# Kernel tuning notes

Measured on AMD Instinct MI355X. Metric: run time of the kernel, lower is better.

## Reference

```python
import jax, jax.numpy as jnp
import numpy as np

B, N, NPOINT, NSAMPLE = 8, 8192, 2048, 64
RADIUS = 0.2
C_IN = 64  # input feature channels; mlp[0]=64 -> 67 after use_xyz concat


def setup_inputs() -> dict:
    key = jax.random.key(0)
    ks = jax.random.split(key, 12)
    xyz = jax.random.uniform(ks[0], (B, N, 3), dtype=jnp.float32)
    features = jax.random.normal(ks[1], (B, N, C_IN), dtype=jnp.float32)
    inds = jax.random.randint(ks[2], (B, NPOINT), 0, N, dtype=jnp.int32)

    def mkw(k, cin, cout):
        return jax.random.normal(k, (cin, cout), jnp.float32) * (1.0 / np.sqrt(cin).astype(np.float32))

    w0 = mkw(ks[3], C_IN + 3, 64)
    w1 = mkw(ks[4], 64, 64)
    w2 = mkw(ks[5], 64, 128)
    # BN (inference) folded into per-channel scale/shift
    s0 = 1.0 + 0.1 * jax.random.normal(ks[6], (64,), jnp.float32)
    t0 = 0.1 * jax.random.normal(ks[7], (64,), jnp.float32)
    s1 = 1.0 + 0.1 * jax.random.normal(ks[8], (64,), jnp.float32)
    t1 = 0.1 * jax.random.normal(ks[9], (64,), jnp.float32)
    s2 = 1.0 + 0.1 * jax.random.normal(ks[10], (128,), jnp.float32)
    t2 = 0.1 * jax.random.normal(ks[11], (128,), jnp.float32)
    return dict(xyz=xyz, features=features, inds=inds,
                w0=w0, s0=s0, t0=t0, w1=w1, s1=s1, t1=t1, w2=w2, s2=s2, t2=t2)


def _ball_query(xyz, new_xyz):
    """First NSAMPLE point indices within RADIUS of each query; pad by repeating
    the first hit (matches CUDA ball_query semantics). xyz:(B,N,3) new_xyz:(B,S,3)."""
    nn = jnp.sum(xyz * xyz, axis=-1)            # (B,N)
    qq = jnp.sum(new_xyz * new_xyz, axis=-1)    # (B,S)
    d2 = qq[:, :, None] + nn[:, None, :] - 2.0 * jnp.einsum('bsc,bnc->bsn', new_xyz, xyz)
    within = d2 < (RADIUS * RADIUS)
    ar = jnp.arange(N, dtype=jnp.int32)
    keyed = jnp.where(within, ar[None, None, :], N)   # out-of-radius -> sentinel N
    keyed = jnp.sort(keyed, axis=-1)[:, :, :NSAMPLE]  # first hits in point order
    idx = jnp.where(keyed == N, keyed[:, :, :1], keyed)
    return jnp.minimum(idx, N - 1)


_gather = jax.vmap(lambda pts, i: pts[i])  # (N,C),(M,) -> (M,C) per batch


def reference(xyz, features, inds, w0, s0, t0, w1, s1, t1, w2, s2, t2):
    new_xyz = _gather(xyz, inds)                              # (B,S,3)
    idx = _ball_query(xyz, new_xyz)                           # (B,S,ns)
    flat = idx.reshape(B, NPOINT * NSAMPLE)
    g_xyz = _gather(xyz, flat).reshape(B, NPOINT, NSAMPLE, 3)
    g_xyz = (g_xyz - new_xyz[:, :, None, :]) / RADIUS         # normalize_xyz
    g_feat = _gather(features, flat).reshape(B, NPOINT, NSAMPLE, C_IN)
    x = jnp.concatenate([g_xyz, g_feat], axis=-1)             # (B,S,ns,C+3)
    for wgt, s, t in ((w0, s0, t0), (w1, s1, t1), (w2, s2, t2)):
        x = jax.nn.relu(jnp.einsum('bpsc,cd->bpsd', x, wgt) * s + t)
    new_features = jnp.max(x, axis=2)                         # max-pool over nsample
    return new_xyz, new_features, inds, idx
```

## Files before the change

kernel.cpp:

```cpp
#include <hip/hip_runtime.h>

#define BB 8
#define NN 8192
#define NPOINT 2048
#define NSAMPLE 64
#define CIN 64
#define RADIUS 0.2f
#define R2 (RADIUS * RADIUS)

#define OFF_NEWXYZ 0
#define OFF_FEAT (BB * NPOINT * 3)
#define OFF_INDS (OFF_FEAT + BB * NPOINT * 128)
#define OFF_IDX (OFF_INDS + BB * NPOINT)

typedef _Float16 half8 __attribute__((ext_vector_type(8)));
typedef _Float16 half4 __attribute__((ext_vector_type(4)));
typedef __fp16 f16x2 __attribute__((ext_vector_type(2)));
typedef float floatx16 __attribute__((ext_vector_type(16)));

#define P0 88
#define P1 72
#define X_LOC 0
#define H_LOC (64 * P0)
#define XH_WAVE (64 * P0 + 64 * P1)
#define WT0_S 0
#define WT1_S (64 * P0)
#define WT2_S (64 * P0 + 64 * P1)

#define QPW 8

__global__ __launch_bounds__(256) void ballq_kernel(
    const float* __restrict__ xyz, const int* __restrict__ inds,
    float* __restrict__ out) {
  __shared__ int sidx[4][2][NSAMPLE];
  const int wave = (blockIdx.x * 256 + threadIdx.x) >> 6;
  const int lane = threadIdx.x & 63;
  const int wid = threadIdx.x >> 6;
  const int q0 = wave * 2, q1 = q0 + 1;
  const int b = q0 >> 11;

  const float* xb = xyz + (size_t)b * NN * 3;
  const int i0 = inds[q0], i1 = inds[q1];
  const float c0x = xb[i0 * 3 + 0], c0y = xb[i0 * 3 + 1], c0z = xb[i0 * 3 + 2];
  const float c1x = xb[i1 * 3 + 0], c1y = xb[i1 * 3 + 1], c1z = xb[i1 * 3 + 2];

  if (lane < 2) {
    const int qq_ = lane ? q1 : q0;
    const int ii = lane ? i1 : i0;
    out[OFF_NEWXYZ + (size_t)qq_ * 3 + 0] = lane ? c1x : c0x;
    out[OFF_NEWXYZ + (size_t)qq_ * 3 + 1] = lane ? c1y : c0y;
    out[OFF_NEWXYZ + (size_t)qq_ * 3 + 2] = lane ? c1z : c0z;
    out[OFF_INDS + qq_] = (float)ii;
  }

  const float qq0 = c0x * c0x + c0y * c0y + c0z * c0z;
  const float qq1 = c1x * c1x + c1y * c1y + c1z * c1z;

  int cnt0 = 0, cnt1 = 0;
  float ax[4], ay[4], az[4];
#pragma unroll
  for (int k = 0; k < 4; ++k) {
    const float* p = xb + (size_t)(k * 64 + lane) * 3;
    ax[k] = p[0];
    ay[k] = p[1];
    az[k] = p[2];
  }
  for (int j0 = 0; j0 < NN; j0 += 256) {
    float bx[4] = {0}, by[4] = {0}, bz[4] = {0};
    const int jn = j0 + 256;
    if (jn < NN) {
#pragma unroll
      for (int k = 0; k < 4; ++k) {
        const float* p = xb + (size_t)(jn + k * 64 + lane) * 3;
        bx[k] = p[0];
        by[k] = p[1];
        bz[k] = p[2];
      }
    }
#pragma unroll
    for (int k = 0; k < 4; ++k) {
      const int j = j0 + k * 64 + lane;
      const float nn_ = ax[k] * ax[k] + ay[k] * ay[k] + az[k] * az[k];
      const float dot0 = c0x * ax[k] + c0y * ay[k] + c0z * az[k];
      const float dot1 = c1x * ax[k] + c1y * ay[k] + c1z * az[k];
      const bool hit0 = (qq0 + nn_ - 2.0f * dot0) < R2;
      const bool hit1 = (qq1 + nn_ - 2.0f * dot1) < R2;
      const unsigned long long m0 = __ballot(hit0);
      const unsigned long long m1 = __ballot(hit1);
      if (hit0) {
        const int pos = cnt0 + (int)__popcll(m0 & ((1ull << lane) - 1ull));
        if (pos < NSAMPLE) sidx[wid][0][pos] = j;
      }
      if (hit1) {
        const int pos = cnt1 + (int)__popcll(m1 & ((1ull << lane) - 1ull));
        if (pos < NSAMPLE) sidx[wid][1][pos] = j;
      }
      cnt0 += (int)__popcll(m0);
      cnt1 += (int)__popcll(m1);
    }
    if (cnt0 >= NSAMPLE && cnt1 >= NSAMPLE) break;
#pragma unroll
    for (int k = 0; k < 4; ++k) {
      ax[k] = bx[k];
      ay[k] = by[k];
      az[k] = bz[k];
    }
  }
  const int v0 = sidx[wid][0][lane < cnt0 ? lane : 0];
  out[OFF_IDX + (size_t)q0 * NSAMPLE + lane] = (float)v0;
  const int v1 = sidx[wid][1][lane < cnt1 ? lane : 0];
  out[OFF_IDX + (size_t)q1 * NSAMPLE + lane] = (float)v1;
}

__global__ __launch_bounds__(128, 2) void mlp_mfma(
    const float* __restrict__ xyz, const float* __restrict__ features,
    const int* __restrict__ inds,
    const float* __restrict__ w0, const float* __restrict__ s0,
    const float* __restrict__ t0, const float* __restrict__ w1,
    const float* __restrict__ s1, const float* __restrict__ t1,
    const float* __restrict__ w2, const float* __restrict__ s2,
    const float* __restrict__ t2, float* __restrict__ out) {
  __shared__ _Float16 sm[2 * XH_WAVE];
  const int tid = threadIdx.x;
  const int w = tid >> 6;
  const int l = tid & 63;
  const int l31 = l & 31;
  const int h5 = l >> 5;
  const int koff = h5 * 8;

  {
    const int d = tid >> 1, hf = tid & 1;
    const float sd0 = s0[d], td0 = t0[d], sd1 = s1[d];
#pragma unroll
    for (int j = 0; j < 44; ++j) {
      const int c = hf * 44 + j;
      float v = 0.0f;
      if (c < 64) v = w0[(3 + c) * 64 + d] * sd0;
      else if (c < 67) v = w0[(c - 64) * 64 + d] * sd0;
      else if (c == 67) v = td0;
      sm[WT0_S + d * P0 + c] = (_Float16)v;
    }
#pragma unroll
    for (int j = 0; j < 32; ++j) {
      const int c = hf * 32 + j;
      sm[WT1_S + d * P1 + c] = (_Float16)(w1[c * 64 + d] * sd1);
    }
    const int ch = tid;
    const float sch = s2[ch];
#pragma unroll
    for (int c = 0; c < 64; ++c)
      sm[WT2_S + ch * P1 + c] = (_Float16)(w2[c * 128 + ch] * sch);
  }
  __syncthreads();

  half8 b0f[2][5], b1f[2][4], b2f[4][4];
#pragma unroll
  for (int nt = 0; nt < 2; ++nt)
#pragma unroll
    for (int ks = 0; ks < 5; ++ks)
      b0f[nt][ks] =
          *(const half8*)&sm[WT0_S + (nt * 32 + l31) * P0 + ks * 16 + koff];
#pragma unroll
  for (int nt = 0; nt < 2; ++nt)
#pragma unroll
    for (int ks = 0; ks < 4; ++ks)
      b1f[nt][ks] =
          *(const half8*)&sm[WT1_S + (nt * 32 + l31) * P1 + ks * 16 + koff];
#pragma unroll
  for (int ct = 0; ct < 4; ++ct)
#pragma unroll
    for (int ks = 0; ks < 4; ++ks)
      b2f[ct][ks] =
          *(const half8*)&sm[WT2_S + (ct * 32 + l31) * P1 + ks * 16 + koff];
  const float t1v0 = t1[l31];
  const float t1v1 = t1[32 + l31];
  float t2v[4];
#pragma unroll
  for (int ct = 0; ct < 4; ++ct) t2v[ct] = t2[ct * 32 + l31];
  __syncthreads();

  _Float16* xbuf = sm + w * XH_WAVE + X_LOC;
  _Float16* hbuf = sm + w * XH_WAVE + H_LOC;
  {
    half8 z = {};
    *(half8*)&xbuf[l * P0 + 72] = z;
  }

  const int wq0 = (blockIdx.x * 2 + w) * QPW;
  const int b = wq0 >> 11;
  const float* xb = xyz + (size_t)b * NN * 3;
  const float* fbase = features + (size_t)b * NN * CIN;

  int myidx = (int)out[OFF_IDX + (size_t)wq0 * NSAMPLE + l];
  int indv = inds[wq0];
  float cx = xb[indv * 3 + 0], cy = xb[indv * 3 + 1], cz = xb[indv * 3 + 2];
  float ppx = xb[myidx * 3 + 0], ppy = xb[myidx * 3 + 1],
        ppz = xb[myidx * 3 + 2];

#pragma unroll 1
  for (int qi = 0; qi < QPW; ++qi) {
    const int q = wq0 + qi;
    const int nq = (qi + 1 < QPW) ? q + 1 : q;

    float4 g[16];
#pragma unroll
    for (int i = 0; i < 16; ++i) {
      const int s = (l >> 2) + 16 * (i & 3);
      const int c = (l & 3) + 4 * (i >> 2);
      const int sidx = __shfl(myidx, s, 64);
      g[i] = *(const float4*)(fbase + (size_t)sidx * CIN + 4 * c);
    }
    const float fni = out[OFF_IDX + (size_t)nq * NSAMPLE + l];
    const int nindv = inds[nq];

#pragma unroll
    for (int i = 0; i < 16; ++i) {
      const int s = (l >> 2) + 16 * (i & 3);
      const int c = (l & 3) + 4 * (i >> 2);
      union {
        half4 v;
        f16x2 p[2];
      } hv;
      hv.p[0] = __builtin_amdgcn_cvt_pkrtz(g[i].x, g[i].y);
      hv.p[1] = __builtin_amdgcn_cvt_pkrtz(g[i].z, g[i].w);
      *(half4*)&xbuf[s * P0 + 4 * c] = hv.v;
    }
    {
      union {
        half8 v;
        f16x2 p[4];
      } xv;
      xv.p[0] =
          __builtin_amdgcn_cvt_pkrtz((ppx - cx) * 5.0f, (ppy - cy) * 5.0f);
      xv.p[1] = __builtin_amdgcn_cvt_pkrtz((ppz - cz) * 5.0f, 1.0f);
      xv.p[2] = __builtin_amdgcn_cvt_pkrtz(0.0f, 0.0f);
      xv.p[3] = __builtin_amdgcn_cvt_pkrtz(0.0f, 0.0f);
      *(half8*)&xbuf[l * P0 + 64] = xv.v;
    }

    {
      half8 xa[2][5];
#pragma unroll
      for (int st = 0; st < 2; ++st)
#pragma unroll
        for (int ks = 0; ks < 5; ++ks)
          xa[st][ks] =
              *(const half8*)&xbuf[(st * 32 + l31) * P0 + ks * 16 + koff];
#pragma unroll
      for (int nt = 0; nt < 2; ++nt)
#pragma unroll
        for (int st = 0; st < 2; ++st) {
          floatx16 acc;
#pragma unroll
          for (int i = 0; i < 16; ++i) acc[i] = 0.0f;
#pragma unroll
          for (int ks = 0; ks < 5; ++ks)
            acc = __builtin_amdgcn_mfma_f32_32x32x16_f16(xa[st][ks],
                                                         b0f[nt][ks], acc,
                                                         0, 0, 0);
#pragma unroll
          for (int reg = 0; reg < 16; ++reg) {
            const int row = st * 32 + (reg & 3) + 8 * (reg >> 2) + 4 * h5;
            hbuf[row * P1 + nt * 32 + l31] = (_Float16)fmaxf(acc[reg], 0.0f);
          }
        }
    }

    const int nidxs = (int)fni;
    const float ncx = xb[nindv * 3 + 0];
    const float ncy = xb[nindv * 3 + 1];
    const float ncz = xb[nindv * 3 + 2];
    const float nppx = xb[nidxs * 3 + 0];
    const float nppy = xb[nidxs * 3 + 1];
    const float nppz = xb[nidxs * 3 + 2];

    {
      half8 ha[2][4];
#pragma unroll
      for (int st = 0; st < 2; ++st)
#pragma unroll
        for (int ks = 0; ks < 4; ++ks)
          ha[st][ks] =
              *(const half8*)&hbuf[(st * 32 + l31) * P1 + ks * 16 + koff];
#pragma unroll
      for (int nt = 0; nt < 2; ++nt) {
        const float tt = nt ? t1v1 : t1v0;
#pragma unroll
        for (int st = 0; st < 2; ++st) {
          floatx16 acc;
#pragma unroll
          for (int i = 0; i < 16; ++i) acc[i] = 0.0f;
#pragma unroll
          for (int ks = 0; ks < 4; ++ks)
            acc = __builtin_amdgcn_mfma_f32_32x32x16_f16(ha[st][ks],
                                                         b1f[nt][ks], acc,
                                                         0, 0, 0);
#pragma unroll
          for (int reg = 0; reg < 16; ++reg) {
            const int row = st * 32 + (reg & 3) + 8 * (reg >> 2) + 4 * h5;
            xbuf[row * P0 + nt * 32 + l31] =
                (_Float16)fmaxf(acc[reg] + tt, 0.0f);
          }
        }
      }
    }

    {
      half8 h1a[2][4];
#pragma unroll
      for (int st = 0; st < 2; ++st)
#pragma unroll
        for (int ks = 0; ks < 4; ++ks)
          h1a[st][ks] =
              *(const half8*)&xbuf[(st * 32 + l31) * P0 + ks * 16 + koff];
#pragma unroll
      for (int ct = 0; ct < 4; ++ct) {
        floatx16 aA, aB;
#pragma unroll
        for (int i = 0; i < 16; ++i) {
          aA[i] = 0.0f;
          aB[i] = 0.0f;
        }
#pragma unroll
        for (int ks = 0; ks < 4; ++ks) {
          aA = __builtin_amdgcn_mfma_f32_32x32x16_f16(h1a[0][ks], b2f[ct][ks],
                                                      aA, 0, 0, 0);
          aB = __builtin_amdgcn_mfma_f32_32x32x16_f16(h1a[1][ks], b2f[ct][ks],
                                                      aB, 0, 0, 0);
        }
        float m = fmaxf(aA[0], aB[0]);
#pragma unroll
        for (int i = 1; i < 16; ++i) m = fmaxf(m, fmaxf(aA[i], aB[i]));
        float v = fmaxf(m + t2v[ct], 0.0f);
        v = fmaxf(v, __shfl_xor(v, 32, 64));
        if (l < 32) out[OFF_FEAT + (size_t)q * 128 + ct * 32 + l] = v;
      }
    }

    myidx = nidxs;
    cx = ncx; cy = ncy; cz = ncz;
    ppx = nppx; ppy = nppy; ppz = nppz;
  }
}

extern "C" void kernel_launch(void* const* d_in, const int* in_sizes, int n_in,
                              void* d_out, int out_size, void* d_ws,
                              size_t ws_size, hipStream_t stream) {
  const float* xyz = (const float*)d_in[0];
  const float* features = (const float*)d_in[1];
  const int* inds = (const int*)d_in[2];
  const float* w0 = (const float*)d_in[3];
  const float* s0 = (const float*)d_in[4];
  const float* t0 = (const float*)d_in[5];
  const float* w1 = (const float*)d_in[6];
  const float* s1 = (const float*)d_in[7];
  const float* t1 = (const float*)d_in[8];
  const float* w2 = (const float*)d_in[9];
  const float* s2 = (const float*)d_in[10];
  const float* t2 = (const float*)d_in[11];
  float* out = (float*)d_out;

  const int nquery = BB * NPOINT;
  ballq_kernel<<<nquery / 8, 256, 0, stream>>>(xyz, inds, out);
  mlp_mfma<<<nquery / (2 * QPW), 128, 0, stream>>>(
      xyz, features, inds, w0, s0, t0, w1, s1, t1, w2, s2, t2, out);
}
```

Measured before the change: 174.0 us.

## Software-pipeline feature gather across MLP layers and double-buffer ball-query loads

The MLP kernel now issues the next query's feature gather in two halves during the layer-1 and layer-2 MFMA work. It writes those features into the x buffer after layer-2 operands are loaded into registers, so gather latency overlaps tensor-core compute instead of stalling at the start of each iteration. The ball-query loop is restructured into an A/B ping-pong buffer of 512 points per iteration, which removes the per-iteration register copies and prefetches further ahead. The costs are more registers under launch_bounds(128,2) and a subtle reuse of xbuf that depends on the layer-2 operands being read first.

```diff
diff --git a/kernel.cpp b/kernel.cpp
--- a/kernel.cpp
+++ b/kernel.cpp
@@ -57,55 +57,61 @@
   const float qq1 = c1x * c1x + c1y * c1y + c1z * c1z;
 
   int cnt0 = 0, cnt1 = 0;
-  float ax[4], ay[4], az[4];
+  float Ax[4], Ay[4], Az[4], Bx[4], By[4], Bz[4];
 #pragma unroll
   for (int k = 0; k < 4; ++k) {
     const float* p = xb + (size_t)(k * 64 + lane) * 3;
-    ax[k] = p[0];
-    ay[k] = p[1];
-    az[k] = p[2];
-  }
-  for (int j0 = 0; j0 < NN; j0 += 256) {
-    float bx[4] = {0}, by[4] = {0}, bz[4] = {0};
-    const int jn = j0 + 256;
-    if (jn < NN) {
+    Ax[k] = p[0]; Ay[k] = p[1]; Az[k] = p[2];
+    const float* p2 = xb + (size_t)(256 + k * 64 + lane) * 3;
+    Bx[k] = p2[0]; By[k] = p2[1]; Bz[k] = p2[2];
+  }
+
+#define BALLQ_STEP(PX, PY, PZ, JBASE, K)                                     \
+  {                                                                          \
+    const int j = (JBASE) + (K)*64 + lane;                                   \
+    const float nn_ =                                                        \
+        PX[K] * PX[K] + PY[K] * PY[K] + PZ[K] * PZ[K];                       \
+    const float dot0 = c0x * PX[K] + c0y * PY[K] + c0z * PZ[K];              \
+    const float dot1 = c1x * PX[K] + c1y * PY[K] + c1z * PZ[K];              \
+    const bool hit0 = (qq0 + nn_ - 2.0f * dot0) < R2;                        \
+    const bool hit1 = (qq1 + nn_ - 2.0f * dot1) < R2;                        \
+    const unsigned long long m0 = __ballot(hit0);                            \
+    const unsigned long long m1 = __ballot(hit1);                            \
+    if (hit0) {                                                              \
+      const int pos = cnt0 + (int)__popcll(m0 & ((1ull << lane) - 1ull));    \
+      if (pos < NSAMPLE) sidx[wid][0][pos] = j;                              \
+    }                                                                        \
+    if (hit1) {                                                              \
+      const int pos = cnt1 + (int)__popcll(m1 & ((1ull << lane) - 1ull));    \
+      if (pos < NSAMPLE) sidx[wid][1][pos] = j;                              \
+    }                                                                        \
+    cnt0 += (int)__popcll(m0);                                               \
+    cnt1 += (int)__popcll(m1);                                               \
+  }
+
+  for (int j0 = 0; j0 < NN; j0 += 512) {
+#pragma unroll
+    for (int k = 0; k < 4; ++k) BALLQ_STEP(Ax, Ay, Az, j0, k)
+    if (j0 + 512 < NN) {
 #pragma unroll
       for (int k = 0; k < 4; ++k) {
-        const float* p = xb + (size_t)(jn + k * 64 + lane) * 3;
-        bx[k] = p[0];
-        by[k] = p[1];
-        bz[k] = p[2];
-      }
-    }
-#pragma unroll
-    for (int k = 0; k < 4; ++k) {
-      const int j = j0 + k * 64 + lane;
-      const float nn_ = ax[k] * ax[k] + ay[k] * ay[k] + az[k] * az[k];
-      const float dot0 = c0x * ax[k] + c0y * ay[k] + c0z * az[k];
-      const float dot1 = c1x * ax[k] + c1y * ay[k] + c1z * az[k];
-      const bool hit0 = (qq0 + nn_ - 2.0f * dot0) < R2;
-      const bool hit1 = (qq1 + nn_ - 2.0f * dot1) < R2;
-      const unsigned long long m0 = __ballot(hit0);
-      const unsigned long long m1 = __ballot(hit1);
-      if (hit0) {
-        const int pos = cnt0 + (int)__popcll(m0 & ((1ull << lane) - 1ull));
-        if (pos < NSAMPLE) sidx[wid][0][pos] = j;
-      }
-      if (hit1) {
-        const int pos = cnt1 + (int)__popcll(m1 & ((1ull << lane) - 1ull));
-        if (pos < NSAMPLE) sidx[wid][1][pos] = j;
-      }
-      cnt0 += (int)__popcll(m0);
-      cnt1 += (int)__popcll(m1);
+        const float* p = xb + (size_t)(j0 + 512 + k * 64 + lane) * 3;
+        Ax[k] = p[0]; Ay[k] = p[1]; Az[k] = p[2];
+      }
+    }
+#pragma unroll
+    for (int k = 0; k < 4; ++k) BALLQ_STEP(Bx, By, Bz, j0 + 256, k)
+    if (j0 + 768 < NN) {
+#pragma unroll
+      for (int k = 0; k < 4; ++k) {
+        const float* p = xb + (size_t)(j0 + 768 + k * 64 + lane) * 3;
+        Bx[k] = p[0]; By[k] = p[1]; Bz[k] = p[2];
+      }
     }
     if (cnt0 >= NSAMPLE && cnt1 >= NSAMPLE) break;
-#pragma unroll
-    for (int k = 0; k < 4; ++k) {
-      ax[k] = bx[k];
-      ay[k] = by[k];
-      az[k] = bz[k];
-    }
-  }
+  }
+#undef BALLQ_STEP
+
   const int v0 = sidx[wid][0][lane < cnt0 ? lane : 0];
   out[OFF_IDX + (size_t)q0 * NSAMPLE + lane] = (float)v0;
   const int v1 = sidx[wid][1][lane < cnt1 ? lane : 0];
@@ -191,52 +197,45 @@
   const float* xb = xyz + (size_t)b * NN * 3;
   const float* fbase = features + (size_t)b * NN * CIN;
 
-  int myidx = (int)out[OFF_IDX + (size_t)wq0 * NSAMPLE + l];
-  int indv = inds[wq0];
-  float cx = xb[indv * 3 + 0], cy = xb[indv * 3 + 1], cz = xb[indv * 3 + 2];
-  float ppx = xb[myidx * 3 + 0], ppy = xb[myidx * 3 + 1],
-        ppz = xb[myidx * 3 + 2];
+  {
+    const int idx0 = (int)out[OFF_IDX + (size_t)wq0 * NSAMPLE + l];
+    const int ind0 = inds[wq0];
+    const float cx = xb[ind0 * 3 + 0], cy = xb[ind0 * 3 + 1],
+                cz = xb[ind0 * 3 + 2];
+    const float px = xb[idx0 * 3 + 0], py = xb[idx0 * 3 + 1],
+                pz = xb[idx0 * 3 + 2];
+    float4 g[16];
+#pragma unroll
+    for (int i = 0; i < 16; ++i) {
+      const int s = (l >> 2) + 16 * (i & 3);
+      const int c = (l & 3) + 4 * (i >> 2);
+      const int si = __shfl(idx0, s, 64);
+      g[i] = *(const float4*)(fbase + (size_t)si * CIN + 4 * c);
+    }
+#pragma unroll
+    for (int i = 0; i < 16; ++i) {
+      const int s = (l >> 2) + 16 * (i & 3);
+      const int c = (l & 3) + 4 * (i >> 2);
+      union { half4 v; f16x2 p[2]; } hv;
+      hv.p[0] = __builtin_amdgcn_cvt_pkrtz(g[i].x, g[i].y);
+      hv.p[1] = __builtin_amdgcn_cvt_pkrtz(g[i].z, g[i].w);
+      *(half4*)&xbuf[s * P0 + 4 * c] = hv.v;
+    }
+    union { half8 v; f16x2 p[4]; } xv;
+    xv.p[0] = __builtin_amdgcn_cvt_pkrtz((px - cx) * 5.0f, (py - cy) * 5.0f);
+    xv.p[1] = __builtin_amdgcn_cvt_pkrtz((pz - cz) * 5.0f, 1.0f);
+    xv.p[2] = __builtin_amdgcn_cvt_pkrtz(0.0f, 0.0f);
+    xv.p[3] = __builtin_amdgcn_cvt_pkrtz(0.0f, 0.0f);
+    *(half8*)&xbuf[l * P0 + 64] = xv.v;
+  }
 
 #pragma unroll 1
   for (int qi = 0; qi < QPW; ++qi) {
     const int q = wq0 + qi;
     const int nq = (qi + 1 < QPW) ? q + 1 : q;
 
-    float4 g[16];
-#pragma unroll
-    for (int i = 0; i < 16; ++i) {
-      const int s = (l >> 2) + 16 * (i & 3);
-      const int c = (l & 3) + 4 * (i >> 2);
-      const int sidx = __shfl(myidx, s, 64);
-      g[i] = *(const float4*)(fbase + (size_t)sidx * CIN + 4 * c);
-    }
     const float fni = out[OFF_IDX + (size_t)nq * NSAMPLE + l];
     const int nindv = inds[nq];
-
-#pragma unroll
-    for (int i = 0; i < 16; ++i) {
-      const int s = (l >> 2) + 16 * (i & 3);
-      const int c = (l & 3) + 4 * (i >> 2);
-      union {
-        half4 v;
-        f16x2 p[2];
-      } hv;
-      hv.p[0] = __builtin_amdgcn_cvt_pkrtz(g[i].x, g[i].y);
-      hv.p[1] = __builtin_amdgcn_cvt_pkrtz(g[i].z, g[i].w);
-      *(half4*)&xbuf[s * P0 + 4 * c] = hv.v;
-    }
-    {
-      union {
-        half8 v;
-        f16x2 p[4];
-      } xv;
-      xv.p[0] =
-          __builtin_amdgcn_cvt_pkrtz((ppx - cx) * 5.0f, (ppy - cy) * 5.0f);
-      xv.p[1] = __builtin_amdgcn_cvt_pkrtz((ppz - cz) * 5.0f, 1.0f);
-      xv.p[2] = __builtin_amdgcn_cvt_pkrtz(0.0f, 0.0f);
-      xv.p[3] = __builtin_amdgcn_cvt_pkrtz(0.0f, 0.0f);
-      *(half8*)&xbuf[l * P0 + 64] = xv.v;
-    }
 
     {
       half8 xa[2][5];
@@ -267,6 +266,14 @@
     }
 
     const int nidxs = (int)fni;
+    float4 g1[8];
+#pragma unroll
+    for (int i = 0; i < 8; ++i) {
+      const int s = (l >> 2) + 16 * (i & 3);
+      const int c = (l & 3) + 4 * (i >> 2);
+      const int si = __shfl(nidxs, s, 64);
+      g1[i] = *(const float4*)(fbase + (size_t)si * CIN + 4 * c);
+    }
     const float ncx = xb[nindv * 3 + 0];
     const float ncy = xb[nindv * 3 + 1];
     const float ncz = xb[nindv * 3 + 2];
@@ -305,6 +312,15 @@
       }
     }
 
+    float4 g2[8];
+#pragma unroll
+    for (int i = 8; i < 16; ++i) {
+      const int s = (l >> 2) + 16 * (i & 3);
+      const int c = (l & 3) + 4 * (i >> 2);
+      const int si = __shfl(nidxs, s, 64);
+      g2[i - 8] = *(const float4*)(fbase + (size_t)si * CIN + 4 * c);
+    }
+
     {
       half8 h1a[2][4];
 #pragma unroll
@@ -313,6 +329,35 @@
         for (int ks = 0; ks < 4; ++ks)
           h1a[st][ks] =
               *(const half8*)&xbuf[(st * 32 + l31) * P0 + ks * 16 + koff];
+
+#pragma unroll
+      for (int i = 0; i < 8; ++i) {
+        const int s = (l >> 2) + 16 * (i & 3);
+        const int c = (l & 3) + 4 * (i >> 2);
+        union { half4 v; f16x2 p[2]; } hv;
+        hv.p[0] = __builtin_amdgcn_cvt_pkrtz(g1[i].x, g1[i].y);
+        hv.p[1] = __builtin_amdgcn_cvt_pkrtz(g1[i].z, g1[i].w);
+        *(half4*)&xbuf[s * P0 + 4 * c] = hv.v;
+      }
+#pragma unroll
+      for (int i = 8; i < 16; ++i) {
+        const int s = (l >> 2) + 16 * (i & 3);
+        const int c = (l & 3) + 4 * (i >> 2);
+        union { half4 v; f16x2 p[2]; } hv;
+        hv.p[0] = __builtin_amdgcn_cvt_pkrtz(g2[i - 8].x, g2[i - 8].y);
+        hv.p[1] = __builtin_amdgcn_cvt_pkrtz(g2[i - 8].z, g2[i - 8].w);
+        *(half4*)&xbuf[s * P0 + 4 * c] = hv.v;
+      }
+      {
+        union { half8 v; f16x2 p[4]; } xv;
+        xv.p[0] = __builtin_amdgcn_cvt_pkrtz((nppx - ncx) * 5.0f,
+                                             (nppy - ncy) * 5.0f);
+        xv.p[1] = __builtin_amdgcn_cvt_pkrtz((nppz - ncz) * 5.0f, 1.0f);
+        xv.p[2] = __builtin_amdgcn_cvt_pkrtz(0.0f, 0.0f);
+        xv.p[3] = __builtin_amdgcn_cvt_pkrtz(0.0f, 0.0f);
+        *(half8*)&xbuf[l * P0 + 64] = xv.v;
+      }
+
 #pragma unroll
       for (int ct = 0; ct < 4; ++ct) {
         floatx16 aA, aB;
@@ -336,10 +381,6 @@
         if (l < 32) out[OFF_FEAT + (size_t)q * 128 + ct * 32 + l] = v;
       }
     }
-
-    myidx = nidxs;
-    cx = ncx; cy = ncy; cz = ncz;
-    ppx = nppx; ppy = nppy; ppz = nppz;
   }
 }
 
```

New measurement: 211.0 us. +21.3%, slower.
